# Optimization experiments

Measured on AMD Instinct MI355X. Metric: run time of the kernel, lower is better.

The kernel has to match this reference:

```python
import jax, jax.numpy as jnp
from jax import lax
import numpy as np

DIM = 384
HEADS = 8
B, H, W = 8, 128, 128
_DN = ('NCHW', 'OIHW', 'NCHW')


def setup_inputs() -> dict:
    key = jax.random.key(0)
    ks = jax.random.split(key, 8)
    x = jax.random.normal(ks[0], (B, DIM, H, W), jnp.float32)
    qkv_w = jax.random.normal(ks[1], (3 * DIM, DIM, 1, 1), jnp.float32) * 0.02
    qkv_b = jax.random.normal(ks[2], (3 * DIM,), jnp.float32) * 0.02
    dw_w = jax.random.normal(ks[3], (3 * DIM, 1, 3, 3), jnp.float32) * 0.02
    dw_b = jax.random.normal(ks[4], (3 * DIM,), jnp.float32) * 0.02
    proj_w = jax.random.normal(ks[5], (DIM, DIM, 1, 1), jnp.float32) * 0.02
    proj_b = jax.random.normal(ks[6], (DIM,), jnp.float32) * 0.02
    temperature = jnp.ones((HEADS, 1, 1), jnp.float32)
    return {"x": x, "qkv_w": qkv_w, "qkv_b": qkv_b, "dw_w": dw_w,
            "dw_b": dw_b, "proj_w": proj_w, "proj_b": proj_b,
            "temperature": temperature}


def _l2norm(t, eps=1e-12):
    # F.normalize(t, dim=-1): divide by max(||t||_2, eps)
    n = jnp.sqrt(jnp.sum(t * t, axis=-1, keepdims=True))
    return t / jnp.maximum(n, eps)


def reference(x, qkv_w, qkv_b, dw_w, dw_b, proj_w, proj_b, temperature):
    b, C, h, w = x.shape
    heads = HEADS
    c = C // heads
    hw = h * w
    # 1x1 pointwise qkv conv
    qkv = lax.conv_general_dilated(x, qkv_w, (1, 1), 'VALID',
                                   dimension_numbers=_DN) + qkv_b[None, :, None, None]
    # 3x3 depthwise conv, padding=1
    qkv = lax.conv_general_dilated(qkv, dw_w, (1, 1), ((1, 1), (1, 1)),
                                   feature_group_count=3 * C,
                                   dimension_numbers=_DN) + dw_b[None, :, None, None]
    q, k, v = jnp.split(qkv, 3, axis=1)
    # b (head c) h w -> b head c (h w)
    q = q.reshape(b, heads, c, hw)
    k = k.reshape(b, heads, c, hw)
    v = v.reshape(b, heads, c, hw)
    q = _l2norm(q)
    k = _l2norm(k)
    # processor scales q by temperature*sqrt(hw); SDPA divides by sqrt(hw):
    # net logits = temperature * q_n @ k_n^T  (CxC channel attention per head)
    temp = temperature.reshape(1, heads, 1, 1)
    logits = jnp.einsum('bhcn,bhdn->bhcd', q * temp, k)
    attn = jax.nn.softmax(logits, axis=-1)
    out = jnp.einsum('bhcd,bhdn->bhcn', attn, v)  # [b, heads, c, hw]
    out = out.reshape(b, C, h, w)
    return lax.conv_general_dilated(out, proj_w, (1, 1), 'VALID',
                                    dimension_numbers=_DN) + proj_b[None, :, None, None]
```

## Files before the change

### kernel.cpp

```cpp
#include <hip/hip_runtime.h>
#include <hip/hip_bf16.h>
#include <cstdint>


#define BATCH 8
#define DIM 384
#define HEADS 8
#define CH 48
#define HW 16384
#define C3 1152

typedef __attribute__((ext_vector_type(8))) short bf16x8;
typedef __attribute__((ext_vector_type(8))) unsigned short u16x8;
typedef __attribute__((ext_vector_type(4))) float f32x4;

__device__ __forceinline__ float b2f(ushort b) {
  union { float f; unsigned u; } x; x.u = ((unsigned)b) << 16; return x.f;
}
__device__ __forceinline__ ushort f2b(float f) {
  union { float f; unsigned u; } x; x.f = f;
  unsigned r = x.u + 0x7fffu + ((x.u >> 16) & 1u);
  return (ushort)(r >> 16);
}

__device__ __forceinline__ void async16(const ushort* g, ushort* l) {
  __builtin_amdgcn_global_load_lds(
      (const __attribute__((address_space(1))) unsigned int*)(unsigned long long)(uintptr_t)g,
      (__attribute__((address_space(3))) unsigned int*)(unsigned int)(uintptr_t)l,
      16, 0, 0);
}

__global__ __launch_bounds__(256) void cast_w(const float* __restrict__ s,
                                              ushort* __restrict__ d, int n) {
  int i = (blockIdx.x * 256 + threadIdx.x) * 4;
  if (i + 3 < n) {
    float4 v = *(const float4*)(s + i);
    ushort4 o = make_ushort4(f2b(v.x), f2b(v.y), f2b(v.z), f2b(v.w));
    *(ushort4*)(d + i) = o;
  }
}

template <typename SrcT, int OUT_BF16>
__global__ __launch_bounds__(256, 2) void gemm_px(
    const ushort* __restrict__ A, const SrcT* __restrict__ src,
    const float* __restrict__ bias, void* __restrict__ Cout,
    int M, long Asb, long Ssb, long Csb) {
  constexpr int K = DIM;
  int zb = blockIdx.y;
  int px0 = blockIdx.x * 64;
  const ushort* Ab = A + (size_t)zb * Asb;
  const SrcT* Sb = src + (size_t)zb * Ssb;
  __shared__ __align__(16) ushort Bs[64 * 384];
  __shared__ __align__(16) ushort As[2][128 * 64];
  int tid = threadIdx.x, lane = tid & 63, wid = tid >> 6;
  int wm = wid >> 1, wn = wid & 1;
  int fr = lane & 15, fs = lane >> 4;

  {
    int pix = tid & 63;
    int cg = tid >> 6;
#pragma unroll
    for (int rr = 0; rr < 12; ++rr) {
      int c8 = cg + rr * 4;
      u16x8 pk;
#pragma unroll
      for (int j = 0; j < 8; ++j) {
        int c = c8 * 8 + j;
        if constexpr (sizeof(SrcT) == 4)
          pk[j] = f2b(((const float*)Sb)[(size_t)c * HW + px0 + pix]);
        else
          pk[j] = ((const ushort*)Sb)[(size_t)c * HW + px0 + pix];
      }
      *(u16x8*)&Bs[pix * 384 + ((c8 ^ (pix & 7)) << 3)] = pk;
    }
  }

  auto stageA = [&](int buf, int mt, int k0) {
#pragma unroll
    for (int q = 0; q < 4; ++q) {
      int r = q * 32 + wid * 8 + (lane >> 3);
      int col = ((lane & 7) ^ (r & 7)) * 8;
      async16(Ab + (size_t)(mt * 128 + r) * K + k0 + col,
              &As[buf][(q * 32 + wid * 8) * 64]);
    }
  };

  f32x4 acc[4][2];
  auto compute = [&](int buf, int k0) {
#pragma unroll
    for (int kk = 0; kk < 2; ++kk) {
      bf16x8 af[4], bv[2];
#pragma unroll
      for (int m = 0; m < 4; ++m) {
        int R = wm * 64 + m * 16 + fr;
        int slot = kk * 4 + fs;
        af[m] = *(const bf16x8*)&As[buf][R * 64 + ((slot ^ (R & 7)) << 3)];
      }
#pragma unroll
      for (int n = 0; n < 2; ++n) {
        int P = wn * 32 + n * 16 + fr;
        int gslot = (k0 >> 3) + kk * 4 + fs;
        bv[n] = *(const bf16x8*)&Bs[P * 384 + ((gslot ^ (P & 7)) << 3)];
      }
#pragma unroll
      for (int m = 0; m < 4; ++m)
#pragma unroll
        for (int n = 0; n < 2; ++n)
          acc[m][n] = __builtin_amdgcn_mfma_f32_16x16x32_bf16(af[m], bv[n], acc[m][n], 0, 0, 0);
    }
  };

  const int MT = M >> 7;
  stageA(0, 0, 0);
  __syncthreads();

  for (int mt = 0; mt < MT; ++mt) {
    f32x4 zero = {0.f, 0.f, 0.f, 0.f};
#pragma unroll
    for (int m = 0; m < 4; ++m)
#pragma unroll
      for (int n = 0; n < 2; ++n) acc[m][n] = zero;
#pragma unroll
    for (int t = 0; t < 5; ++t) {
      stageA((t + 1) & 1, mt, (t + 1) * 64);
      __builtin_amdgcn_s_setprio(1);
      compute(t & 1, t * 64);
      __builtin_amdgcn_s_setprio(0);
      __syncthreads();
    }
    if (mt + 1 < MT) stageA(0, mt + 1, 0);
    __builtin_amdgcn_s_setprio(1);
    compute(1, 320);
    __builtin_amdgcn_s_setprio(0);
#pragma unroll
    for (int m = 0; m < 4; ++m)
#pragma unroll
      for (int j = 0; j < 4; ++j) {
        int gr = mt * 128 + wm * 64 + m * 16 + fs * 4 + j;
        float bz = bias[gr];
#pragma unroll
        for (int n = 0; n < 2; ++n) {
          int gc = px0 + wn * 32 + n * 16 + fr;
          float v = acc[m][n][j] + bz;
          if constexpr (OUT_BF16)
            ((ushort*)Cout)[(size_t)zb * Csb + (size_t)gr * HW + gc] = f2b(v);
          else
            ((float*)Cout)[(size_t)zb * Csb + (size_t)gr * HW + gc] = v;
        }
      }
    __syncthreads();
  }
}

__global__ __launch_bounds__(256) void dwconv(
    const ushort* __restrict__ in, const float* __restrict__ w9,
    const float* __restrict__ b9, ushort* __restrict__ out,
    float* __restrict__ sq) {
  int ch = blockIdx.x;
  int b = blockIdx.y;
  const size_t plane = ((size_t)b * C3 + ch) * HW;
  int tid = threadIdx.x, lane = tid & 63;
  int rg = tid >> 4, cg = tid & 15;
  int r0 = rg * 8, c0 = cg * 8;

  float w[9];
#pragma unroll
  for (int i = 0; i < 9; ++i) w[i] = w9[ch * 9 + i];
  float bias = b9[ch];

  float a0[8], a1[8];
#pragma unroll
  for (int c = 0; c < 8; ++c) { a0[c] = 0.f; a1[c] = 0.f; }
  float ss = 0.f;

#pragma unroll
  for (int it = 0; it < 10; ++it) {
    int r = r0 - 1 + it;
    float x[8];
    if ((unsigned)r < 128u) {
      u16x8 raw = *(const u16x8*)(in + plane + (size_t)r * 128 + c0);
#pragma unroll
      for (int c = 0; c < 8; ++c) x[c] = b2f(raw[c]);
    } else {
#pragma unroll
      for (int c = 0; c < 8; ++c) x[c] = 0.f;
    }
    float xl = __shfl(x[7], lane - 1);
    float xr = __shfl(x[0], lane + 1);
    if (cg == 0) xl = 0.f;
    if (cg == 15) xr = 0.f;

    float h0[8], h1[8], h2[8];
#pragma unroll
    for (int c = 0; c < 8; ++c) {
      float l = (c == 0) ? xl : x[c - 1];
      float rt = (c == 7) ? xr : x[c + 1];
      h0[c] = w[0] * l + w[1] * x[c] + w[2] * rt;
      h1[c] = w[3] * l + w[4] * x[c] + w[5] * rt;
      h2[c] = w[6] * l + w[7] * x[c] + w[8] * rt;
    }
    if (it >= 2) {
      int R = r - 1;
      u16x8 pk;
#pragma unroll
      for (int c = 0; c < 8; ++c) {
        float o = a0[c] + h2[c] + bias;
        ss += o * o;
        pk[c] = f2b(o);
      }
      *(u16x8*)(out + plane + (size_t)R * 128 + c0) = pk;
    }
#pragma unroll
    for (int c = 0; c < 8; ++c) { a0[c] = a1[c] + h1[c]; a1[c] = h0[c]; }
  }

  if (ch < 2 * DIM) {
#pragma unroll
    for (int off = 32; off; off >>= 1) ss += __shfl_down(ss, off, 64);
    if (lane == 0) atomicAdd(&sq[b * 2 * DIM + ch], ss);
  }
}

__global__ __launch_bounds__(256) void gram(const ushort* __restrict__ qkvd,
                                            float* __restrict__ G) {
  int chunk = blockIdx.x;
  int bh = blockIdx.y;
  int b = bh >> 3, h = bh & 7;
  int tid = threadIdx.x, lane = tid & 63, wid = tid >> 6;
  const ushort* qbase = qkvd + ((size_t)b * C3 + h * CH) * HW;
  const ushort* kbase = qbase + (size_t)DIM * HW;
  int pix0 = chunk * 1024 + wid * 256;
  int fr = lane & 15, fk = (lane >> 4) * 8;
  f32x4 zero = {0.f, 0.f, 0.f, 0.f};
  f32x4 acc[3][3];
#pragma unroll
  for (int i = 0; i < 3; ++i)
#pragma unroll
    for (int j = 0; j < 3; ++j) acc[i][j] = zero;
#pragma unroll
  for (int it = 0; it < 8; ++it) {
    int pix = pix0 + it * 32 + fk;
    bf16x8 aq[3], bk[3];
#pragma unroll
    for (int mi = 0; mi < 3; ++mi)
      aq[mi] = *(const bf16x8*)(qbase + (size_t)(mi * 16 + fr) * HW + pix);
#pragma unroll
    for (int ni = 0; ni < 3; ++ni)
      bk[ni] = *(const bf16x8*)(kbase + (size_t)(ni * 16 + fr) * HW + pix);
#pragma unroll
    for (int mi = 0; mi < 3; ++mi)
#pragma unroll
      for (int ni = 0; ni < 3; ++ni)
        acc[mi][ni] = __builtin_amdgcn_mfma_f32_16x16x32_bf16(aq[mi], bk[ni], acc[mi][ni], 0, 0, 0);
  }
  __shared__ float gs[CH * CH];
  for (int i = tid; i < CH * CH; i += 256) gs[i] = 0.f;
  __syncthreads();
  int crow = (lane >> 4) * 4, ccol = lane & 15;
#pragma unroll
  for (int mi = 0; mi < 3; ++mi)
#pragma unroll
    for (int ni = 0; ni < 3; ++ni)
#pragma unroll
      for (int j = 0; j < 4; ++j)
        atomicAdd(&gs[(mi * 16 + crow + j) * CH + ni * 16 + ccol], acc[mi][ni][j]);
  __syncthreads();
  float* Gp = G + (size_t)bh * CH * CH;
  for (int i = tid; i < CH * CH; i += 256) atomicAdd(&Gp[i], gs[i]);
}

__global__ void softmax_k(const float* __restrict__ G, const float* __restrict__ sq,
                          const float* __restrict__ temp, float* __restrict__ attn) {
  int bh = blockIdx.x, b = bh >> 3, h = bh & 7;
  int lane = threadIdx.x;
  __shared__ float inq[CH], ink[CH];
  if (lane < CH) {
    inq[lane] = 1.f / fmaxf(sqrtf(sq[b * 2 * DIM + h * CH + lane]), 1e-12f);
    ink[lane] = 1.f / fmaxf(sqrtf(sq[b * 2 * DIM + DIM + h * CH + lane]), 1e-12f);
  }
  __syncthreads();
  if (lane < CH) {
    float t = temp[h] * inq[lane];
    const float* g = G + (size_t)bh * CH * CH + lane * CH;
    float v[CH];
    float mx = -1e30f;
#pragma unroll
    for (int d = 0; d < CH; ++d) { v[d] = t * g[d] * ink[d]; mx = fmaxf(mx, v[d]); }
    float s = 0.f;
#pragma unroll
    for (int d = 0; d < CH; ++d) { v[d] = expf(v[d] - mx); s += v[d]; }
    float inv = 1.f / s;
    float* a = attn + (size_t)bh * CH * CH + lane * CH;
#pragma unroll
    for (int d = 0; d < CH; ++d) a[d] = v[d] * inv;
  }
}

__global__ __launch_bounds__(384) void weff_k(const float* __restrict__ pw,
                                              const float* __restrict__ attn,
                                              ushort* __restrict__ weff) {
  int dg = threadIdx.x;
  int p = blockIdx.x;
  int b = blockIdx.y;
  int h = dg / CH, d = dg - h * CH;
  const float* a = attn + (((size_t)b * HEADS + h) * CH) * CH + d;
  const float* wrow = pw + (size_t)p * DIM + h * CH;
  float s = 0.f;
#pragma unroll
  for (int c = 0; c < CH; ++c) s += wrow[c] * a[c * CH];
  weff[((size_t)b * DIM + p) * DIM + dg] = f2b(s);
}

extern "C" void kernel_launch(void* const* d_in, const int* in_sizes, int n_in,
                              void* d_out, int out_size, void* d_ws, size_t ws_size,
                              hipStream_t stream) {
  const float* x = (const float*)d_in[0];
  const float* qkv_w = (const float*)d_in[1];
  const float* qkv_b = (const float*)d_in[2];
  const float* dw_w = (const float*)d_in[3];
  const float* dw_b = (const float*)d_in[4];
  const float* proj_w = (const float*)d_in[5];
  const float* proj_b = (const float*)d_in[6];
  const float* temp = (const float*)d_in[7];

  const size_t SZ_C1 = (size_t)BATCH * C3 * HW * 2;
  const size_t SZ_WQB = (size_t)C3 * DIM * 2;
  const size_t SZ_SQ = (size_t)BATCH * 2 * DIM * 4;
  const size_t SZ_G = (size_t)BATCH * HEADS * CH * CH * 4;

  const size_t OFF_C1 = 0;
  const size_t OFF_QKVD = OFF_C1 + SZ_C1;
  const size_t OFF_WQB = OFF_QKVD + SZ_C1;
  const size_t OFF_SQ = OFF_WQB + SZ_WQB;
  const size_t OFF_G = OFF_SQ + SZ_SQ;
  const size_t OFF_ATTN = OFF_G + SZ_G;
  const size_t OFF_WEFF = OFF_ATTN + SZ_G;
  const size_t TOTAL = OFF_WEFF + (size_t)BATCH * DIM * DIM * 2;
  if (ws_size < TOTAL) return;

  char* ws = (char*)d_ws;
  ushort* c1 = (ushort*)(ws + OFF_C1);
  ushort* qkvd = (ushort*)(ws + OFF_QKVD);
  ushort* wqb = (ushort*)(ws + OFF_WQB);
  float* sq = (float*)(ws + OFF_SQ);
  float* G = (float*)(ws + OFF_G);
  float* attn = (float*)(ws + OFF_ATTN);
  ushort* weff = (ushort*)(ws + OFF_WEFF);

  hipMemsetAsync(ws + OFF_SQ, 0, SZ_SQ + SZ_G, stream);

  cast_w<<<(C3 * DIM) / 1024, 256, 0, stream>>>(qkv_w, wqb, C3 * DIM);
  gemm_px<float, 1><<<dim3(HW / 64, BATCH), 256, 0, stream>>>(
      wqb, x, qkv_b, (void*)c1, C3, 0L, (long)DIM * HW, (long)C3 * HW);
  dwconv<<<dim3(C3, BATCH), 256, 0, stream>>>(c1, dw_w, dw_b, qkvd, sq);
  gram<<<dim3(16, BATCH * HEADS), 256, 0, stream>>>(qkvd, G);
  softmax_k<<<BATCH * HEADS, 64, 0, stream>>>(G, sq, temp, attn);
  weff_k<<<dim3(DIM, BATCH), 384, 0, stream>>>(proj_w, attn, weff);
  gemm_px<ushort, 0><<<dim3(HW / 64, BATCH), 256, 0, stream>>>(
      weff, qkvd + (size_t)2 * DIM * HW, proj_b, d_out, DIM,
      (long)DIM * DIM, (long)C3 * HW, (long)DIM * HW);
}
```

Baseline: 535.9 us.

## Load GEMM A-fragments directly from global into registers, drop LDS staging

The pixel GEMM no longer stages weight tiles through double-buffered LDS with async loads and block barriers. Each wave now reads its A fragments straight from global memory (L2/L1-cached weights) into registers, software-pipelined one half-step ahead. This frees LDS so launch bounds can ask for 3 blocks per SM instead of 2, and removes the per-k-step __syncthreads. The risks are more global-load latency per wave, redundant weight reads across the two wn waves, and register pressure under the tighter launch bound. The workspace padding was also grown by 1 KB, likely so the last fragment prefetch, which reads one step past the end of the weights, stays inside the allocation.

After: 962.9 us. +79.7%, slower.

```diff
diff --git a/kernel.cpp b/kernel.cpp
--- a/kernel.cpp
+++ b/kernel.cpp
@@ -21,13 +21,6 @@
   union { float f; unsigned u; } x; x.f = f;
   unsigned r = x.u + 0x7fffu + ((x.u >> 16) & 1u);
   return (ushort)(r >> 16);
-}
-
-__device__ __forceinline__ void async16(const ushort* g, ushort* l) {
-  __builtin_amdgcn_global_load_lds(
-      (const __attribute__((address_space(1))) unsigned int*)(unsigned long long)(uintptr_t)g,
-      (__attribute__((address_space(3))) unsigned int*)(unsigned int)(uintptr_t)l,
-      16, 0, 0);
 }
 
 __global__ __launch_bounds__(256) void cast_w(const float* __restrict__ s,
@@ -41,7 +34,7 @@
 }
 
 template <typename SrcT, int OUT_BF16>
-__global__ __launch_bounds__(256, 2) void gemm_px(
+__global__ __launch_bounds__(256, 3) void gemm_px(
     const ushort* __restrict__ A, const SrcT* __restrict__ src,
     const float* __restrict__ bias, void* __restrict__ Cout,
     int M, long Asb, long Ssb, long Csb) {
@@ -51,7 +44,6 @@
   const ushort* Ab = A + (size_t)zb * Asb;
   const SrcT* Sb = src + (size_t)zb * Ssb;
   __shared__ __align__(16) ushort Bs[64 * 384];
-  __shared__ __align__(16) ushort As[2][128 * 64];
   int tid = threadIdx.x, lane = tid & 63, wid = tid >> 6;
   int wm = wid >> 1, wn = wid & 1;
   int fr = lane & 15, fs = lane >> 4;
@@ -74,64 +66,69 @@
       *(u16x8*)&Bs[pix * 384 + ((c8 ^ (pix & 7)) << 3)] = pk;
     }
   }
-
-  auto stageA = [&](int buf, int mt, int k0) {
-#pragma unroll
-    for (int q = 0; q < 4; ++q) {
-      int r = q * 32 + wid * 8 + (lane >> 3);
-      int col = ((lane & 7) ^ (r & 7)) * 8;
-      async16(Ab + (size_t)(mt * 128 + r) * K + k0 + col,
-              &As[buf][(q * 32 + wid * 8) * 64]);
-    }
-  };
-
-  f32x4 acc[4][2];
-  auto compute = [&](int buf, int k0) {
-#pragma unroll
-    for (int kk = 0; kk < 2; ++kk) {
-      bf16x8 af[4], bv[2];
-#pragma unroll
-      for (int m = 0; m < 4; ++m) {
-        int R = wm * 64 + m * 16 + fr;
-        int slot = kk * 4 + fs;
-        af[m] = *(const bf16x8*)&As[buf][R * 64 + ((slot ^ (R & 7)) << 3)];
-      }
+  __syncthreads();
+
+  const int MT = M >> 7;
+  const ushort* Aw = Ab + (size_t)(wm * 64 + fr) * K + (fs << 3);
+
+  for (int mt = 0; mt < MT; ++mt) {
+    const ushort* Am = Aw + (size_t)mt * 128 * K;
+    f32x4 acc[4][2];
+    f32x4 zero = {0.f, 0.f, 0.f, 0.f};
+#pragma unroll
+    for (int m = 0; m < 4; ++m)
+#pragma unroll
+      for (int n = 0; n < 2; ++n) acc[m][n] = zero;
+
+    bf16x8 afA[4], afB[4];
+#pragma unroll
+    for (int m = 0; m < 4; ++m)
+      afA[m] = *(const bf16x8*)(Am + (size_t)m * 16 * K);
+#pragma unroll
+    for (int m = 0; m < 4; ++m)
+      afB[m] = *(const bf16x8*)(Am + (size_t)m * 16 * K + 32);
+
+#pragma unroll 1
+    for (int kp = 0; kp < 6; ++kp) {
+      bf16x8 afN[4], bv[2];
+#pragma unroll
+      for (int m = 0; m < 4; ++m)
+        afN[m] = *(const bf16x8*)(Am + (size_t)m * 16 * K + (kp + 1) * 64);
 #pragma unroll
       for (int n = 0; n < 2; ++n) {
         int P = wn * 32 + n * 16 + fr;
-        int gslot = (k0 >> 3) + kk * 4 + fs;
+        int gslot = kp * 8 + fs;
         bv[n] = *(const bf16x8*)&Bs[P * 384 + ((gslot ^ (P & 7)) << 3)];
       }
+      __builtin_amdgcn_s_setprio(1);
 #pragma unroll
       for (int m = 0; m < 4; ++m)
 #pragma unroll
         for (int n = 0; n < 2; ++n)
-          acc[m][n] = __builtin_amdgcn_mfma_f32_16x16x32_bf16(af[m], bv[n], acc[m][n], 0, 0, 0);
-    }
-  };
-
-  const int MT = M >> 7;
-  stageA(0, 0, 0);
-  __syncthreads();
-
-  for (int mt = 0; mt < MT; ++mt) {
-    f32x4 zero = {0.f, 0.f, 0.f, 0.f};
-#pragma unroll
-    for (int m = 0; m < 4; ++m)
-#pragma unroll
-      for (int n = 0; n < 2; ++n) acc[m][n] = zero;
-#pragma unroll
-    for (int t = 0; t < 5; ++t) {
-      stageA((t + 1) & 1, mt, (t + 1) * 64);
+          acc[m][n] = __builtin_amdgcn_mfma_f32_16x16x32_bf16(afA[m], bv[n], acc[m][n], 0, 0, 0);
+      __builtin_amdgcn_s_setprio(0);
+#pragma unroll
+      for (int m = 0; m < 4; ++m) afA[m] = afN[m];
+#pragma unroll
+      for (int m = 0; m < 4; ++m)
+        afN[m] = *(const bf16x8*)(Am + (size_t)m * 16 * K + (kp + 1) * 64 + 32);
+#pragma unroll
+      for (int n = 0; n < 2; ++n) {
+        int P = wn * 32 + n * 16 + fr;
+        int gslot = kp * 8 + 4 + fs;
+        bv[n] = *(const bf16x8*)&Bs[P * 384 + ((gslot ^ (P & 7)) << 3)];
+      }
       __builtin_amdgcn_s_setprio(1);
-      compute(t & 1, t * 64);
+#pragma unroll
+      for (int m = 0; m < 4; ++m)
+#pragma unroll
+        for (int n = 0; n < 2; ++n)
+          acc[m][n] = __builtin_amdgcn_mfma_f32_16x16x32_bf16(afB[m], bv[n], acc[m][n], 0, 0, 0);
       __builtin_amdgcn_s_setprio(0);
-      __syncthreads();
-    }
-    if (mt + 1 < MT) stageA(0, mt + 1, 0);
-    __builtin_amdgcn_s_setprio(1);
-    compute(1, 320);
-    __builtin_amdgcn_s_setprio(0);
+#pragma unroll
+      for (int m = 0; m < 4; ++m) afB[m] = afN[m];
+    }
+
 #pragma unroll
     for (int m = 0; m < 4; ++m)
 #pragma unroll
@@ -148,7 +145,6 @@
             ((float*)Cout)[(size_t)zb * Csb + (size_t)gr * HW + gc] = v;
         }
       }
-    __syncthreads();
   }
 }
 
@@ -335,7 +331,7 @@
   const size_t OFF_G = OFF_SQ + SZ_SQ;
   const size_t OFF_ATTN = OFF_G + SZ_G;
   const size_t OFF_WEFF = OFF_ATTN + SZ_G;
-  const size_t TOTAL = OFF_WEFF + (size_t)BATCH * DIM * DIM * 2;
+  const size_t TOTAL = OFF_WEFF + (size_t)BATCH * DIM * DIM * 2 + 1024;
   if (ws_size < TOTAL) return;
 
   char* ws = (char*)d_ws;
```
